# Optimization experiments

Measured on AMD Instinct MI355X. Metric: run time of the kernel, lower is better.

Reference implementation:

```python
import jax, jax.numpy as jnp
import numpy as np

NUM_HEADS = 16
HEAD_SIZE = 64
N_EMBD = 1024
BLOCK_SIZE = 2048
B, T = 4, 2048


def setup_inputs() -> dict:
    key = jax.random.key(0)
    ks = jax.random.split(key, 6)
    scale = (N_EMBD * NUM_HEADS) ** (-0.5)
    x = jax.random.normal(ks[0], (B, T, N_EMBD), dtype=jnp.float32)
    Wk = jax.random.normal(ks[1], (NUM_HEADS, N_EMBD, HEAD_SIZE), dtype=jnp.float32) * scale
    Wq = jax.random.normal(ks[2], (NUM_HEADS, N_EMBD, HEAD_SIZE), dtype=jnp.float32) * scale
    Wv = jax.random.normal(ks[3], (NUM_HEADS, N_EMBD, HEAD_SIZE), dtype=jnp.float32) * scale
    proj_w = jax.random.normal(ks[4], (N_EMBD, N_EMBD), dtype=jnp.float32) * (N_EMBD ** -0.5)
    proj_b = jax.random.normal(ks[5], (N_EMBD,), dtype=jnp.float32) * 0.01
    return {"x": x, "Wk": Wk, "Wq": Wq, "Wv": Wv, "proj_w": proj_w, "proj_b": proj_b}


def reference(x, Wk, Wq, Wv, proj_w, proj_b):
    Bsz, Tlen, C = x.shape
    # per-head projections: x [b,t,c] @ W [h,c,d] -> [b,h,t,d]
    q = jnp.einsum('btc,hcd->bhtd', x, Wq)
    k = jnp.einsum('btc,hcd->bhtd', x, Wk)
    v = jnp.einsum('btc,hcd->bhtd', x, Wv)
    wei = jnp.einsum('bhtd,bhsd->bhts', q, k) * (HEAD_SIZE ** -0.5)
    causal = jnp.tril(jnp.ones((Tlen, Tlen), dtype=bool))  # [T,T]
    wei = jnp.where(causal[None, None, :, :], wei, -jnp.inf)
    wei = jax.nn.softmax(wei, axis=-1)
    out = jnp.einsum('bhts,bhsd->bhtd', wei, v)
    out = out.transpose(0, 2, 1, 3).reshape(Bsz, Tlen, NUM_HEADS * HEAD_SIZE)
    out = out @ proj_w.T + proj_b  # nn.Linear: x W^T + b
    return out
```

## Files before the change

### kernel.cpp

```cpp
#include <hip/hip_runtime.h>
#include <hip/hip_bf16.h>

#define BB 4
#define TT 2048
#define CC 1024
#define HH 16
#define DD 64
#define MM (BB * TT)
#define NN_QKV 3072

typedef __attribute__((ext_vector_type(8))) short short8;
typedef __attribute__((ext_vector_type(4))) short short4v;
typedef __attribute__((ext_vector_type(4))) int i32x4;
typedef __attribute__((ext_vector_type(4))) float f32x4;
typedef __attribute__((ext_vector_type(16))) float f32x16;

static __device__ __forceinline__ float exp2_hw(float x) {
  return __builtin_amdgcn_exp2f(x);
}

static __device__ __forceinline__ short f2bf(float f) {
  __hip_bfloat16 h = __float2bfloat16(f);
  short s;
  __builtin_memcpy(&s, &h, 2);
  return s;
}

static __device__ __forceinline__ unsigned int pack2(float a, float b) {
  unsigned int lo = (unsigned short)f2bf(a);
  unsigned int hi = (unsigned short)f2bf(b);
  return lo | (hi << 16);
}

static __device__ __forceinline__ f32x16 zero16() {
  f32x16 z;
#pragma unroll
  for (int i = 0; i < 16; ++i) z[i] = 0.f;
  return z;
}

static __device__ __forceinline__ void gld16(const void* g, void* l) {
  __builtin_amdgcn_global_load_lds(
      (const __attribute__((address_space(1))) unsigned int*)g,
      (__attribute__((address_space(3))) unsigned int*)l, 16, 0, 0);
}

__global__ __launch_bounds__(256) void cvt8_kernel(const float* __restrict__ in,
                                                   short* __restrict__ out, int n8) {
  int i = blockIdx.x * 256 + threadIdx.x;
  if (i >= n8) return;
  const float4 a = ((const float4*)in)[i * 2];
  const float4 b = ((const float4*)in)[i * 2 + 1];
  short8 o;
  o[0] = f2bf(a.x); o[1] = f2bf(a.y); o[2] = f2bf(a.z); o[3] = f2bf(a.w);
  o[4] = f2bf(b.x); o[5] = f2bf(b.y); o[6] = f2bf(b.z); o[7] = f2bf(b.w);
  ((short8*)out)[i] = o;
}

__global__ __launch_bounds__(256) void cvtw_kernel(
    const float* __restrict__ Wq, const float* __restrict__ Wk,
    const float* __restrict__ Wv, short* __restrict__ Wt) {
  __shared__ float tile[64][65];
  const int tid = threadIdx.x;
  const int h = blockIdx.x;
  const int c0 = blockIdx.y * 64;
  const int sel = blockIdx.z;
  const float* W = (sel == 0) ? Wq : (sel == 1) ? Wk : Wv;

#pragma unroll
  for (int it = 0; it < 16; ++it) {
    int e = it * 256 + tid;
    int cc = e >> 6, d = e & 63;
    tile[d][cc] = W[((size_t)h * CC + c0 + cc) * DD + d];
  }
  __syncthreads();
#pragma unroll
  for (int it = 0; it < 16; ++it) {
    int e = it * 256 + tid;
    int d = e >> 6, cc = e & 63;
    Wt[((size_t)((sel * 16 + h) * 64 + d)) * CC + c0 + cc] = f2bf(tile[d][cc]);
  }
}

template <int MODE>
__global__ __launch_bounds__(256) void mfma_gemm_kernel(
    const short* __restrict__ A, const short* __restrict__ Bt,
    const float* __restrict__ bias,
    __hip_bfloat16* __restrict__ Oq, __hip_bfloat16* __restrict__ Ok,
    __hip_bfloat16* __restrict__ Ov, float* __restrict__ Of) {
  __shared__ __align__(16) short Als[128 * 32];
  __shared__ __align__(16) short Bls[128 * 32];

  const int tid = threadIdx.x;
  const int w = tid >> 6, l = tid & 63;
  const int lg = l >> 4, ll = l & 15;
  const int wr = w >> 1, wc = w & 1;
  const int m0 = blockIdx.x * 128;
  const int n0 = blockIdx.y * 128;

  const int row0 = tid >> 2, kc0 = (tid & 3) * 8;
  const int row1 = (tid + 256) >> 2, kc1 = (tid & 3) * 8;

  f32x4 acc[4][4] = {};

  for (int kt = 0; kt < CC; kt += 32) {
    __syncthreads();
    gld16(A + (size_t)(m0 + row0) * CC + kt + kc0, (char*)Als + w * 1024);
    gld16(A + (size_t)(m0 + row1) * CC + kt + kc1, (char*)Als + 4096 + w * 1024);
    gld16(Bt + (size_t)(n0 + row0) * CC + kt + kc0, (char*)Bls + w * 1024);
    gld16(Bt + (size_t)(n0 + row1) * CC + kt + kc1, (char*)Bls + 4096 + w * 1024);
    __syncthreads();

    short8 af[4], bfr[4];
#pragma unroll
    for (int i = 0; i < 4; ++i)
      af[i] = *(const short8*)&Als[(wr * 64 + i * 16 + ll) * 32 + lg * 8];
#pragma unroll
    for (int j = 0; j < 4; ++j)
      bfr[j] = *(const short8*)&Bls[(wc * 64 + j * 16 + ll) * 32 + lg * 8];
#pragma unroll
    for (int i = 0; i < 4; ++i)
#pragma unroll
      for (int j = 0; j < 4; ++j)
        acc[i][j] = __builtin_amdgcn_mfma_f32_16x16x32_bf16(af[i], bfr[j], acc[i][j], 0, 0, 0);
  }

  if (MODE == 0) {
    const int b = m0 >> 11;
#pragma unroll
    for (int j = 0; j < 4; ++j) {
      const int nbase = n0 + wc * 64 + j * 16;
      const int sel = nbase >> 10;
      const int h = (nbase >> 6) & 15;
      const int d = (nbase & 63) + ll;
      __hip_bfloat16* O = (sel == 0) ? Oq : (sel == 1) ? Ok : Ov;
      const float sc = (sel == 0) ? 0.18033688011112042f : 1.0f;
#pragma unroll
      for (int i = 0; i < 4; ++i) {
#pragma unroll
        for (int r = 0; r < 4; ++r) {
          const int t = (m0 + wr * 64 + i * 16 + lg * 4 + r) & (TT - 1);
          O[(((size_t)b * HH + h) * TT + t) * DD + d] = __float2bfloat16(acc[i][j][r] * sc);
        }
      }
    }
  } else {
#pragma unroll
    for (int j = 0; j < 4; ++j) {
      const int n = n0 + wc * 64 + j * 16 + ll;
      const float bv = bias[n];
#pragma unroll
      for (int i = 0; i < 4; ++i) {
#pragma unroll
        for (int r = 0; r < 4; ++r) {
          const int m = m0 + wr * 64 + i * 16 + lg * 4 + r;
          Of[(size_t)m * CC + n] = acc[i][j][r] + bv;
        }
      }
    }
  }
}

__global__ __launch_bounds__(256) void attn32_kernel(
    const __hip_bfloat16* __restrict__ qg, const __hip_bfloat16* __restrict__ kg,
    const __hip_bfloat16* __restrict__ vg, __hip_bfloat16* __restrict__ att) {
  __shared__ __align__(16) char Ks[2 * 64 * 128];
  __shared__ __align__(16) char Vt[2 * 64 * 128];

  const int tid = threadIdx.x;
  const int w = tid >> 6, l = tid & 63;
  const int l31 = l & 31, hi = l >> 5;
  const int h = blockIdx.y, b = blockIdx.z;
  const size_t base = ((size_t)b * HH + h) * TT * DD;

  const short* Kg = (const short*)kg + base;
  const short* Vg = (const short*)vg + base;
  const int kr0 = w * 8 + (l >> 3);
  const int kr1 = kr0 + 32;
  const int kc = l & 7;
  const int vs = tid >> 2;
  const int vd0 = (tid & 3) * 16;

#pragma unroll 1
  for (int grp = 0; grp < 2; ++grp) {
    const int qt = (grp == 0) ? (15 - (int)blockIdx.x) : (int)blockIdx.x;
    const int q0w = qt * 128 + w * 32;
    const int myq = q0w + l31;

    const short* Qp = (const short*)qg + base + (size_t)myq * DD;
    const short8 qf0 = *(const short8*)(Qp + 0 + hi * 8);
    const short8 qf1 = *(const short8*)(Qp + 16 + hi * 8);
    const short8 qf2 = *(const short8*)(Qp + 32 + hi * 8);
    const short8 qf3 = *(const short8*)(Qp + 48 + hi * 8);

    f32x16 o0 = zero16(), o1 = zero16();
    float m = -INFINITY, lsum = 0.f;

    const int NT = 2 * qt + 2;
    int cur = 0;

    {
      gld16(Kg + (size_t)kr0 * DD + ((kc ^ (kr0 & 7)) * 8), Ks + w * 1024);
      gld16(Kg + (size_t)kr1 * DD + ((kc ^ (kr1 & 7)) * 8), Ks + 4096 + w * 1024);
      const short8 va = *(const short8*)(Vg + (size_t)vs * DD + vd0);
      const short8 vb = *(const short8*)(Vg + (size_t)vs * DD + vd0 + 8);
#pragma unroll
      for (int e = 0; e < 8; ++e) {
        const int d = vd0 + e;
        *(short*)(Vt + d * 128 + ((vs * 2) ^ ((d & 7) << 4))) = va[e];
      }
#pragma unroll
      for (int e = 0; e < 8; ++e) {
        const int d = vd0 + 8 + e;
        *(short*)(Vt + d * 128 + ((vs * 2) ^ ((d & 7) << 4))) = vb[e];
      }
      __syncthreads();
    }

#pragma unroll 1
    for (int t = 0; t < NT; ++t) {
      const int sb = t * 64;
      const int nxt = cur ^ 1;
      const bool haveNext = (t + 1 < NT);

      short8 nva = {}, nvb = {};
      if (haveNext) {
        const int sb2 = sb + 64;
        gld16(Kg + (size_t)(sb2 + kr0) * DD + ((kc ^ (kr0 & 7)) * 8),
              Ks + nxt * 8192 + w * 1024);
        gld16(Kg + (size_t)(sb2 + kr1) * DD + ((kc ^ (kr1 & 7)) * 8),
              Ks + nxt * 8192 + 4096 + w * 1024);
        nva = *(const short8*)(Vg + (size_t)(sb2 + vs) * DD + vd0);
        nvb = *(const short8*)(Vg + (size_t)(sb2 + vs) * DD + vd0 + 8);
      }

      if (sb <= q0w + 31) {
        const char* Ksb = Ks + cur * 8192;
        const char* Vtb = Vt + cur * 8192;
#pragma unroll
        for (int ks = 0; ks < 2; ++ks) {
          const int sbh = sb + ks * 32;
          if (sbh > q0w + 31) continue;

          const int krow = ks * 32 + l31;
          const char* Kr = Ksb + krow * 128;
          const int rsz = (krow & 7) << 4;
          const short8 kf0 = *(const short8*)(Kr + ((0 * 32 + hi * 16) ^ rsz));
          const short8 kf1 = *(const short8*)(Kr + ((1 * 32 + hi * 16) ^ rsz));
          const short8 kf2 = *(const short8*)(Kr + ((2 * 32 + hi * 16) ^ rsz));
          const short8 kf3 = *(const short8*)(Kr + ((3 * 32 + hi * 16) ^ rsz));
          f32x16 sT = zero16();
          __builtin_amdgcn_s_setprio(1);
          sT = __builtin_amdgcn_mfma_f32_32x32x16_bf16(kf0, qf0, sT, 0, 0, 0);
          sT = __builtin_amdgcn_mfma_f32_32x32x16_bf16(kf1, qf1, sT, 0, 0, 0);
          sT = __builtin_amdgcn_mfma_f32_32x32x16_bf16(kf2, qf2, sT, 0, 0, 0);
          sT = __builtin_amdgcn_mfma_f32_32x32x16_bf16(kf3, qf3, sT, 0, 0, 0);
          __builtin_amdgcn_s_setprio(0);

          float p[16];
          if (sbh == q0w) {
#pragma unroll
            for (int r = 0; r < 16; ++r) {
              const int sg = sbh + (r & 3) + 8 * (r >> 2) + 4 * hi;
              p[r] = (sg > myq) ? -INFINITY : sT[r];
            }
          } else {
#pragma unroll
            for (int r = 0; r < 16; ++r) p[r] = sT[r];
          }

          float tmax = p[0];
#pragma unroll
          for (int r = 1; r < 16; ++r) tmax = fmaxf(tmax, p[r]);
          tmax = fmaxf(tmax, __shfl_xor(tmax, 32));
          if (!__all(tmax <= m + 8.f)) {
            const float mn = fmaxf(m, tmax);
            const float corr = exp2_hw(m - mn);
            m = mn;
            lsum *= corr;
            o0 *= corr;
            o1 *= corr;
          }
          float ps = 0.f;
#pragma unroll
          for (int r = 0; r < 16; ++r) {
            p[r] = exp2_hw(p[r] - m);
            ps += p[r];
          }
          ps += __shfl_xor(ps, 32);
          lsum += ps;

          unsigned int W[4][2], X[4][2];
#pragma unroll
          for (int qd = 0; qd < 4; ++qd) {
            W[qd][0] = pack2(p[4 * qd + 0], p[4 * qd + 1]);
            W[qd][1] = pack2(p[4 * qd + 2], p[4 * qd + 3]);
            X[qd][0] = __shfl_xor((int)W[qd][0], 32);
            X[qd][1] = __shfl_xor((int)W[qd][1], 32);
          }

#pragma unroll
          for (int kst = 0; kst < 2; ++kst) {
            union { i32x4 i; short8 s; } A;
            A.i[0] = hi ? (int)X[2 * kst + 1][0] : (int)W[2 * kst][0];
            A.i[1] = hi ? (int)X[2 * kst + 1][1] : (int)W[2 * kst][1];
            A.i[2] = hi ? (int)W[2 * kst + 1][0] : (int)X[2 * kst][0];
            A.i[3] = hi ? (int)W[2 * kst + 1][1] : (int)X[2 * kst][1];
            const int kb = (ks * 32 + kst * 16 + hi * 8) * 2;
            const int r0 = l31, r1 = 32 + l31;
            const short8 vf0 = *(const short8*)(Vtb + r0 * 128 + (kb ^ ((r0 & 7) << 4)));
            const short8 vf1 = *(const short8*)(Vtb + r1 * 128 + (kb ^ ((r1 & 7) << 4)));
            __builtin_amdgcn_s_setprio(1);
            o0 = __builtin_amdgcn_mfma_f32_32x32x16_bf16(vf0, A.s, o0, 0, 0, 0);
            o1 = __builtin_amdgcn_mfma_f32_32x32x16_bf16(vf1, A.s, o1, 0, 0, 0);
            __builtin_amdgcn_s_setprio(0);
          }
        }
      }

      if (haveNext) {
        char* Vb = Vt + nxt * 8192;
#pragma unroll
        for (int e = 0; e < 8; ++e) {
          const int d = vd0 + e;
          *(short*)(Vb + d * 128 + ((vs * 2) ^ ((d & 7) << 4))) = nva[e];
        }
#pragma unroll
        for (int e = 0; e < 8; ++e) {
          const int d = vd0 + 8 + e;
          *(short*)(Vb + d * 128 + ((vs * 2) ^ ((d & 7) << 4))) = nvb[e];
        }
      }
      __syncthreads();
      cur = nxt;
    }

    const float inv = 1.0f / lsum;
    short* orow = (short*)att + ((size_t)b * TT + myq) * CC + h * DD;
#pragma unroll
    for (int j = 0; j < 4; ++j) {
      short4v s0, s1;
#pragma unroll
      for (int i = 0; i < 4; ++i) {
        s0[i] = f2bf(o0[4 * j + i] * inv);
        s1[i] = f2bf(o1[4 * j + i] * inv);
      }
      *(short4v*)(orow + 8 * j + 4 * hi) = s0;
      *(short4v*)(orow + 32 + 8 * j + 4 * hi) = s1;
    }
  }
}

extern "C" void kernel_launch(void* const* d_in, const int* in_sizes, int n_in,
                              void* d_out, int out_size, void* d_ws, size_t ws_size,
                              hipStream_t stream) {
  const float* x  = (const float*)d_in[0];
  const float* Wk = (const float*)d_in[1];
  const float* Wq = (const float*)d_in[2];
  const float* Wv = (const float*)d_in[3];
  const float* pw = (const float*)d_in[4];
  const float* pb = (const float*)d_in[5];
  float* out = (float*)d_out;

  const size_t QE = (size_t)BB * HH * TT * DD;
  __hip_bfloat16* q   = (__hip_bfloat16*)d_ws;
  __hip_bfloat16* k   = q + QE;
  __hip_bfloat16* v   = k + QE;
  short* xbf          = (short*)(v + QE);
  __hip_bfloat16* att = (__hip_bfloat16*)xbf;
  short* Wt           = xbf + QE;
  short* pwbf         = Wt;

  cvt8_kernel<<<(MM * CC / 8 + 255) / 256, 256, 0, stream>>>(x, xbf, MM * CC / 8);
  cvtw_kernel<<<dim3(HH, CC / 64, 3), 256, 0, stream>>>(Wq, Wk, Wv, Wt);
  mfma_gemm_kernel<0><<<dim3(MM / 128, NN_QKV / 128), 256, 0, stream>>>(
      xbf, Wt, nullptr, q, k, v, nullptr);
  attn32_kernel<<<dim3(8, HH, BB), 256, 0, stream>>>(q, k, v, att);
  cvt8_kernel<<<(CC * CC / 8 + 255) / 256, 256, 0, stream>>>(pw, pwbf, CC * CC / 8);
  mfma_gemm_kernel<1><<<dim3(MM / 128, CC / 128), 256, 0, stream>>>(
      (const short*)att, pwbf, pb, nullptr, nullptr, nullptr, out);
}
```

Before: 194.9 us.

## Process both causal query tiles concurrently with 512-thread attention blocks

The attention kernel previously handled its two paired query tiles (a late tile and an early tile) one after the other with 4 waves. It now launches 8 waves per block, with waves 0-3 taking the long tile and waves 4-7 the short one, sharing a single K/V stream sized to the long tile. Each thread now loads half as much K/V per step, and the two query groups run concurrently rather than back to back. In exchange, the short-tile waves sit idle at barriers once their causal range ends, and the larger blocks may lower occupancy per CU.

```diff
diff --git a/kernel.cpp b/kernel.cpp
--- a/kernel.cpp
+++ b/kernel.cpp
@@ -161,7 +161,7 @@
   }
 }
 
-__global__ __launch_bounds__(256) void attn32_kernel(
+__global__ __launch_bounds__(512) void attn32_kernel(
     const __hip_bfloat16* __restrict__ qg, const __hip_bfloat16* __restrict__ kg,
     const __hip_bfloat16* __restrict__ vg, __hip_bfloat16* __restrict__ att) {
   __shared__ __align__(16) char Ks[2 * 64 * 128];
@@ -173,181 +173,163 @@
   const int h = blockIdx.y, b = blockIdx.z;
   const size_t base = ((size_t)b * HH + h) * TT * DD;
 
+  const int w4 = w & 3;
+  const int qt = (w >> 2) ? (int)blockIdx.x : (15 - (int)blockIdx.x);
+  const int q0w = qt * 128 + w4 * 32;
+  const int myq = q0w + l31;
+
   const short* Kg = (const short*)kg + base;
   const short* Vg = (const short*)vg + base;
-  const int kr0 = w * 8 + (l >> 3);
-  const int kr1 = kr0 + 32;
-  const int kc = l & 7;
-  const int vs = tid >> 2;
-  const int vd0 = (tid & 3) * 16;
+  const int kr = tid >> 3;
+  const int kc = tid & 7;
+  const int vs = tid >> 3;
+  const int vd0 = (tid & 7) * 8;
+
+  const short* Qp = (const short*)qg + base + (size_t)myq * DD;
+  const short8 qf0 = *(const short8*)(Qp + 0 + hi * 8);
+  const short8 qf1 = *(const short8*)(Qp + 16 + hi * 8);
+  const short8 qf2 = *(const short8*)(Qp + 32 + hi * 8);
+  const short8 qf3 = *(const short8*)(Qp + 48 + hi * 8);
+
+  f32x16 o0 = zero16(), o1 = zero16();
+  float m = -INFINITY, lsum = 0.f;
+
+  const int NT = 2 * (15 - (int)blockIdx.x) + 2;
+  int cur = 0;
+
+  {
+    gld16(Kg + (size_t)kr * DD + ((kc ^ (kr & 7)) * 8), Ks + w * 1024);
+    const short8 va = *(const short8*)(Vg + (size_t)vs * DD + vd0);
+#pragma unroll
+    for (int e = 0; e < 8; ++e) {
+      const int d = vd0 + e;
+      *(short*)(Vt + d * 128 + ((vs * 2) ^ ((d & 7) << 4))) = va[e];
+    }
+    __syncthreads();
+  }
 
 #pragma unroll 1
-  for (int grp = 0; grp < 2; ++grp) {
-    const int qt = (grp == 0) ? (15 - (int)blockIdx.x) : (int)blockIdx.x;
-    const int q0w = qt * 128 + w * 32;
-    const int myq = q0w + l31;
-
-    const short* Qp = (const short*)qg + base + (size_t)myq * DD;
-    const short8 qf0 = *(const short8*)(Qp + 0 + hi * 8);
-    const short8 qf1 = *(const short8*)(Qp + 16 + hi * 8);
-    const short8 qf2 = *(const short8*)(Qp + 32 + hi * 8);
-    const short8 qf3 = *(const short8*)(Qp + 48 + hi * 8);
-
-    f32x16 o0 = zero16(), o1 = zero16();
-    float m = -INFINITY, lsum = 0.f;
-
-    const int NT = 2 * qt + 2;
-    int cur = 0;
-
-    {
-      gld16(Kg + (size_t)kr0 * DD + ((kc ^ (kr0 & 7)) * 8), Ks + w * 1024);
-      gld16(Kg + (size_t)kr1 * DD + ((kc ^ (kr1 & 7)) * 8), Ks + 4096 + w * 1024);
-      const short8 va = *(const short8*)(Vg + (size_t)vs * DD + vd0);
-      const short8 vb = *(const short8*)(Vg + (size_t)vs * DD + vd0 + 8);
+  for (int t = 0; t < NT; ++t) {
+    const int sb = t * 64;
+    const int nxt = cur ^ 1;
+    const bool haveNext = (t + 1 < NT);
+
+    short8 nva = {};
+    if (haveNext) {
+      const int sb2 = sb + 64;
+      gld16(Kg + (size_t)(sb2 + kr) * DD + ((kc ^ (kr & 7)) * 8),
+            Ks + nxt * 8192 + w * 1024);
+      nva = *(const short8*)(Vg + (size_t)(sb2 + vs) * DD + vd0);
+    }
+
+    if (sb <= q0w + 31) {
+      const char* Ksb = Ks + cur * 8192;
+      const char* Vtb = Vt + cur * 8192;
+#pragma unroll
+      for (int ks = 0; ks < 2; ++ks) {
+        const int sbh = sb + ks * 32;
+        if (sbh > q0w + 31) continue;
+
+        const int krow = ks * 32 + l31;
+        const char* Kr = Ksb + krow * 128;
+        const int rsz = (krow & 7) << 4;
+        const short8 kf0 = *(const short8*)(Kr + ((0 * 32 + hi * 16) ^ rsz));
+        const short8 kf1 = *(const short8*)(Kr + ((1 * 32 + hi * 16) ^ rsz));
+        const short8 kf2 = *(const short8*)(Kr + ((2 * 32 + hi * 16) ^ rsz));
+        const short8 kf3 = *(const short8*)(Kr + ((3 * 32 + hi * 16) ^ rsz));
+        f32x16 sT = zero16();
+        __builtin_amdgcn_s_setprio(1);
+        sT = __builtin_amdgcn_mfma_f32_32x32x16_bf16(kf0, qf0, sT, 0, 0, 0);
+        sT = __builtin_amdgcn_mfma_f32_32x32x16_bf16(kf1, qf1, sT, 0, 0, 0);
+        sT = __builtin_amdgcn_mfma_f32_32x32x16_bf16(kf2, qf2, sT, 0, 0, 0);
+        sT = __builtin_amdgcn_mfma_f32_32x32x16_bf16(kf3, qf3, sT, 0, 0, 0);
+        __builtin_amdgcn_s_setprio(0);
+
+        float p[16];
+        if (sbh == q0w) {
+#pragma unroll
+          for (int r = 0; r < 16; ++r) {
+            const int sg = sbh + (r & 3) + 8 * (r >> 2) + 4 * hi;
+            p[r] = (sg > myq) ? -INFINITY : sT[r];
+          }
+        } else {
+#pragma unroll
+          for (int r = 0; r < 16; ++r) p[r] = sT[r];
+        }
+
+        float tmax = p[0];
+#pragma unroll
+        for (int r = 1; r < 16; ++r) tmax = fmaxf(tmax, p[r]);
+        tmax = fmaxf(tmax, __shfl_xor(tmax, 32));
+        if (!__all(tmax <= m + 8.f)) {
+          const float mn = fmaxf(m, tmax);
+          const float corr = exp2_hw(m - mn);
+          m = mn;
+          lsum *= corr;
+          o0 *= corr;
+          o1 *= corr;
+        }
+        float ps = 0.f;
+#pragma unroll
+        for (int r = 0; r < 16; ++r) {
+          p[r] = exp2_hw(p[r] - m);
+          ps += p[r];
+        }
+        ps += __shfl_xor(ps, 32);
+        lsum += ps;
+
+        unsigned int W[4][2], X[4][2];
+#pragma unroll
+        for (int qd = 0; qd < 4; ++qd) {
+          W[qd][0] = pack2(p[4 * qd + 0], p[4 * qd + 1]);
+          W[qd][1] = pack2(p[4 * qd + 2], p[4 * qd + 3]);
+          X[qd][0] = __shfl_xor((int)W[qd][0], 32);
+          X[qd][1] = __shfl_xor((int)W[qd][1], 32);
+        }
+
+#pragma unroll
+        for (int kst = 0; kst < 2; ++kst) {
+          union { i32x4 i; short8 s; } A;
+          A.i[0] = hi ? (int)X[2 * kst + 1][0] : (int)W[2 * kst][0];
+          A.i[1] = hi ? (int)X[2 * kst + 1][1] : (int)W[2 * kst][1];
+          A.i[2] = hi ? (int)W[2 * kst + 1][0] : (int)X[2 * kst][0];
+          A.i[3] = hi ? (int)W[2 * kst + 1][1] : (int)X[2 * kst][1];
+          const int kb = (ks * 32 + kst * 16 + hi * 8) * 2;
+          const int r0 = l31, r1 = 32 + l31;
+          const short8 vf0 = *(const short8*)(Vtb + r0 * 128 + (kb ^ ((r0 & 7) << 4)));
+          const short8 vf1 = *(const short8*)(Vtb + r1 * 128 + (kb ^ ((r1 & 7) << 4)));
+          __builtin_amdgcn_s_setprio(1);
+          o0 = __builtin_amdgcn_mfma_f32_32x32x16_bf16(vf0, A.s, o0, 0, 0, 0);
+          o1 = __builtin_amdgcn_mfma_f32_32x32x16_bf16(vf1, A.s, o1, 0, 0, 0);
+          __builtin_amdgcn_s_setprio(0);
+        }
+      }
+    }
+
+    if (haveNext) {
+      char* Vb = Vt + nxt * 8192;
 #pragma unroll
       for (int e = 0; e < 8; ++e) {
         const int d = vd0 + e;
-        *(short*)(Vt + d * 128 + ((vs * 2) ^ ((d & 7) << 4))) = va[e];
+        *(short*)(Vb + d * 128 + ((vs * 2) ^ ((d & 7) << 4))) = nva[e];
       }
-#pragma unroll
-      for (int e = 0; e < 8; ++e) {
-        const int d = vd0 + 8 + e;
-        *(short*)(Vt + d * 128 + ((vs * 2) ^ ((d & 7) << 4))) = vb[e];
-      }
-      __syncthreads();
-    }
-
-#pragma unroll 1
-    for (int t = 0; t < NT; ++t) {
-      const int sb = t * 64;
-      const int nxt = cur ^ 1;
-      const bool haveNext = (t + 1 < NT);
-
-      short8 nva = {}, nvb = {};
-      if (haveNext) {
-        const int sb2 = sb + 64;
-        gld16(Kg + (size_t)(sb2 + kr0) * DD + ((kc ^ (kr0 & 7)) * 8),
-              Ks + nxt * 8192 + w * 1024);
-        gld16(Kg + (size_t)(sb2 + kr1) * DD + ((kc ^ (kr1 & 7)) * 8),
-              Ks + nxt * 8192 + 4096 + w * 1024);
-        nva = *(const short8*)(Vg + (size_t)(sb2 + vs) * DD + vd0);
-        nvb = *(const short8*)(Vg + (size_t)(sb2 + vs) * DD + vd0 + 8);
-      }
-
-      if (sb <= q0w + 31) {
-        const char* Ksb = Ks + cur * 8192;
-        const char* Vtb = Vt + cur * 8192;
-#pragma unroll
-        for (int ks = 0; ks < 2; ++ks) {
-          const int sbh = sb + ks * 32;
-          if (sbh > q0w + 31) continue;
-
-          const int krow = ks * 32 + l31;
-          const char* Kr = Ksb + krow * 128;
-          const int rsz = (krow & 7) << 4;
-          const short8 kf0 = *(const short8*)(Kr + ((0 * 32 + hi * 16) ^ rsz));
-          const short8 kf1 = *(const short8*)(Kr + ((1 * 32 + hi * 16) ^ rsz));
-          const short8 kf2 = *(const short8*)(Kr + ((2 * 32 + hi * 16) ^ rsz));
-          const short8 kf3 = *(const short8*)(Kr + ((3 * 32 + hi * 16) ^ rsz));
-          f32x16 sT = zero16();
-          __builtin_amdgcn_s_setprio(1);
-          sT = __builtin_amdgcn_mfma_f32_32x32x16_bf16(kf0, qf0, sT, 0, 0, 0);
-          sT = __builtin_amdgcn_mfma_f32_32x32x16_bf16(kf1, qf1, sT, 0, 0, 0);
-          sT = __builtin_amdgcn_mfma_f32_32x32x16_bf16(kf2, qf2, sT, 0, 0, 0);
-          sT = __builtin_amdgcn_mfma_f32_32x32x16_bf16(kf3, qf3, sT, 0, 0, 0);
-          __builtin_amdgcn_s_setprio(0);
-
-          float p[16];
-          if (sbh == q0w) {
-#pragma unroll
-            for (int r = 0; r < 16; ++r) {
-              const int sg = sbh + (r & 3) + 8 * (r >> 2) + 4 * hi;
-              p[r] = (sg > myq) ? -INFINITY : sT[r];
-            }
-          } else {
-#pragma unroll
-            for (int r = 0; r < 16; ++r) p[r] = sT[r];
-          }
-
-          float tmax = p[0];
-#pragma unroll
-          for (int r = 1; r < 16; ++r) tmax = fmaxf(tmax, p[r]);
-          tmax = fmaxf(tmax, __shfl_xor(tmax, 32));
-          if (!__all(tmax <= m + 8.f)) {
-            const float mn = fmaxf(m, tmax);
-            const float corr = exp2_hw(m - mn);
-            m = mn;
-            lsum *= corr;
-            o0 *= corr;
-            o1 *= corr;
-          }
-          float ps = 0.f;
-#pragma unroll
-          for (int r = 0; r < 16; ++r) {
-            p[r] = exp2_hw(p[r] - m);
-            ps += p[r];
-          }
-          ps += __shfl_xor(ps, 32);
-          lsum += ps;
-
-          unsigned int W[4][2], X[4][2];
-#pragma unroll
-          for (int qd = 0; qd < 4; ++qd) {
-            W[qd][0] = pack2(p[4 * qd + 0], p[4 * qd + 1]);
-            W[qd][1] = pack2(p[4 * qd + 2], p[4 * qd + 3]);
-            X[qd][0] = __shfl_xor((int)W[qd][0], 32);
-            X[qd][1] = __shfl_xor((int)W[qd][1], 32);
-          }
-
-#pragma unroll
-          for (int kst = 0; kst < 2; ++kst) {
-            union { i32x4 i; short8 s; } A;
-            A.i[0] = hi ? (int)X[2 * kst + 1][0] : (int)W[2 * kst][0];
-            A.i[1] = hi ? (int)X[2 * kst + 1][1] : (int)W[2 * kst][1];
-            A.i[2] = hi ? (int)W[2 * kst + 1][0] : (int)X[2 * kst][0];
-            A.i[3] = hi ? (int)W[2 * kst + 1][1] : (int)X[2 * kst][1];
-            const int kb = (ks * 32 + kst * 16 + hi * 8) * 2;
-            const int r0 = l31, r1 = 32 + l31;
-            const short8 vf0 = *(const short8*)(Vtb + r0 * 128 + (kb ^ ((r0 & 7) << 4)));
-            const short8 vf1 = *(const short8*)(Vtb + r1 * 128 + (kb ^ ((r1 & 7) << 4)));
-            __builtin_amdgcn_s_setprio(1);
-            o0 = __builtin_amdgcn_mfma_f32_32x32x16_bf16(vf0, A.s, o0, 0, 0, 0);
-            o1 = __builtin_amdgcn_mfma_f32_32x32x16_bf16(vf1, A.s, o1, 0, 0, 0);
-            __builtin_amdgcn_s_setprio(0);
-          }
-        }
-      }
-
-      if (haveNext) {
-        char* Vb = Vt + nxt * 8192;
-#pragma unroll
-        for (int e = 0; e < 8; ++e) {
-          const int d = vd0 + e;
-          *(short*)(Vb + d * 128 + ((vs * 2) ^ ((d & 7) << 4))) = nva[e];
-        }
-#pragma unroll
-        for (int e = 0; e < 8; ++e) {
-          const int d = vd0 + 8 + e;
-          *(short*)(Vb + d * 128 + ((vs * 2) ^ ((d & 7) << 4))) = nvb[e];
-        }
-      }
-      __syncthreads();
-      cur = nxt;
-    }
-
-    const float inv = 1.0f / lsum;
-    short* orow = (short*)att + ((size_t)b * TT + myq) * CC + h * DD;
-#pragma unroll
-    for (int j = 0; j < 4; ++j) {
-      short4v s0, s1;
-#pragma unroll
-      for (int i = 0; i < 4; ++i) {
-        s0[i] = f2bf(o0[4 * j + i] * inv);
-        s1[i] = f2bf(o1[4 * j + i] * inv);
-      }
-      *(short4v*)(orow + 8 * j + 4 * hi) = s0;
-      *(short4v*)(orow + 32 + 8 * j + 4 * hi) = s1;
-    }
+    }
+    __syncthreads();
+    cur = nxt;
+  }
+
+  const float inv = 1.0f / lsum;
+  short* orow = (short*)att + ((size_t)b * TT + myq) * CC + h * DD;
+#pragma unroll
+  for (int j = 0; j < 4; ++j) {
+    short4v s0, s1;
+#pragma unroll
+    for (int i = 0; i < 4; ++i) {
+      s0[i] = f2bf(o0[4 * j + i] * inv);
+      s1[i] = f2bf(o1[4 * j + i] * inv);
+    }
+    *(short4v*)(orow + 8 * j + 4 * hi) = s0;
+    *(short4v*)(orow + 32 + 8 * j + 4 * hi) = s1;
   }
 }
 
@@ -375,7 +357,7 @@
   cvtw_kernel<<<dim3(HH, CC / 64, 3), 256, 0, stream>>>(Wq, Wk, Wv, Wt);
   mfma_gemm_kernel<0><<<dim3(MM / 128, NN_QKV / 128), 256, 0, stream>>>(
       xbf, Wt, nullptr, q, k, v, nullptr);
-  attn32_kernel<<<dim3(8, HH, BB), 256, 0, stream>>>(q, k, v, att);
+  attn32_kernel<<<dim3(8, HH, BB), 512, 0, stream>>>(q, k, v, att);
   cvt8_kernel<<<(CC * CC / 8 + 255) / 256, 256, 0, stream>>>(pw, pwbf, CC * CC / 8);
   mfma_gemm_kernel<1><<<dim3(MM / 128, CC / 128), 256, 0, stream>>>(
       (const short*)att, pwbf, pb, nullptr, nullptr, nullptr, out);
```

Measured after the change: 188.1 us. 3.5% less time.
